# Performance work log

Hardware: AMD Instinct MI355X
Metric: run time of the kernel (lower is better)

The kernel has to match this reference:

```python
import jax, jax.numpy as jnp
import numpy as np

B, CIN, COUT, T, F = 8, 64, 64, 512, 161
KH, KW = 3, 3
PAD_H, PAD_W = 1, 1
STRIDE_H, STRIDE_W = 1, 1
DIL_H, DIL_W = 1, 1


def setup_inputs() -> dict:
    key = jax.random.key(0)
    k1, k2, k3 = jax.random.split(key, 3)
    x = jax.random.normal(k1, (B, CIN, T, F), dtype=jnp.float32)
    # kernel: [out_ch, in_ch, kernels(freq), kH, kW]
    kernel = jax.random.normal(k2, (COUT, CIN, F, KH, KW), dtype=jnp.float32) * 0.05
    bias = jax.random.normal(k3, (1, COUT, 1, F), dtype=jnp.float32) * 0.05
    return {"x": x, "kernel": kernel, "bias": bias}


def reference(x, kernel, bias):
    # Frequency-varying conv: out[b,o,t,f] = sum_{i,m,n} xp[b,i,t*sH+m*dH, f*sW+n*dW] * kernel[o,i,f,m,n] + bias
    xp = jnp.pad(x, ((0, 0), (0, 0), (PAD_H, PAD_H), (PAD_W, PAD_W)))
    Hp, Wp = xp.shape[-2], xp.shape[-1]
    out_t = (Hp - ((KH - 1) * DIL_H + 1)) // STRIDE_H + 1
    out_f = (Wp - ((KW - 1) * DIL_W + 1)) // STRIDE_W + 1  # == F == kernels
    out = jnp.zeros((x.shape[0], kernel.shape[0], out_t, out_f), dtype=x.dtype)
    # Small fixed loop over the 3x3 window; avoids materializing [B,C,T,F,3,3] patches.
    for m in range(KH):
        for n in range(KW):
            xs = xp[:, :,
                    m * DIL_H : m * DIL_H + out_t * STRIDE_H : STRIDE_H,
                    n * DIL_W : n * DIL_W + out_f * STRIDE_W : STRIDE_W]  # [B,Cin,T,F]
            out = out + jnp.einsum('bitf,oif->botf', xs, kernel[:, :, :, m, n])
    out = out + bias
    return out
```

## Files before the change

kernel.cpp:

```cpp
#include <hip/hip_runtime.h>
#include <hip/hip_bf16.h>

#define CIN   64
#define COUT  64
#define TT    512
#define FF    161
#define KTOT  576
#define TFSTR (TT*FF)
#define FP_   168

#define W2_BYTES  ((size_t)FF*COUT*KTOT*2)
#define X2_BYTES  ((size_t)8*TT*FP_*64*2)
#define TMP_BYTES ((size_t)8*FF*TT*COUT*2)
#define PW_BLOCKS 5796

typedef __bf16 bf16x8 __attribute__((ext_vector_type(8)));
typedef float  f32x4  __attribute__((ext_vector_type(4)));
typedef unsigned short u16x8 __attribute__((ext_vector_type(8)));
typedef unsigned short u16x4 __attribute__((ext_vector_type(4)));
typedef unsigned int   u32x2 __attribute__((ext_vector_type(2)));
typedef float f4u __attribute__((ext_vector_type(4), aligned(4)));

__device__ __forceinline__ unsigned short f2bf(float v) {
    union { float f; unsigned int u; } c; c.f = v;
    unsigned int u = c.u + 0x7FFFu + ((c.u >> 16) & 1u);
    return (unsigned short)(u >> 16);
}
__device__ __forceinline__ float bf2f(unsigned short h) {
    union { unsigned int u; float f; } c; c.u = (unsigned)h << 16;
    return c.f;
}

__global__ __launch_bounds__(256) void prep_fused(
    const float* __restrict__ ksrc, unsigned short* __restrict__ w2,
    const float* __restrict__ x, unsigned short* __restrict__ x2)
{
    __shared__ unsigned short Xs[64][172];
    int bx = blockIdx.x;
    int tid = threadIdx.x;

    if (bx < PW_BLOCKS) {
        int g  = bx*256 + tid;
        int f  = g / 9216;
        int j  = g - f*9216;
        int o  = j / 144;
        int r  = j - o*144;
        int q  = r >> 4;
        int i4 = (r & 15) * 4;
        u16x4 v;
        #pragma unroll
        for (int e = 0; e < 4; ++e)
            v[e] = f2bf(ksrc[((size_t)(o*64 + i4 + e)*FF + f)*9 + q]);
        *(u16x4*)&w2[(size_t)f*36864 + j*4] = v;
        return;
    }

    int bt = bx - PW_BLOCKS;
    int b  = bt >> 9;
    int t  = bt & 511;
    const float* xb = x + (size_t)b*CIN*TFSTR + (size_t)t*FF;
    #pragma unroll
    for (int k = 0; k < 11; ++k) {
        int s = tid + k*256;
        if (s < 2624) {
            int i = s / 41;
            int u = s - i*41;
            const float* p = xb + (size_t)i*TFSTR + 4*u;
            if (u < 40) {
                f4u v = *(const f4u*)p;
                u32x2 pk = { (unsigned)f2bf(v.x) | ((unsigned)f2bf(v.y) << 16),
                             (unsigned)f2bf(v.z) | ((unsigned)f2bf(v.w) << 16) };
                *(u32x2*)&Xs[i][4*u] = pk;
            } else {
                Xs[i][160] = f2bf(*p);
            }
        }
    }
    __syncthreads();
    unsigned short* ob = x2 + (size_t)bt * FP_ * 64;
    #pragma unroll
    for (int k = 0; k < 6; ++k) {
        int s = tid + k*256;
        if (s < 1344) {
            int fp = s >> 3;
            int j  = s & 7;
            u16x8 v = {0,0,0,0,0,0,0,0};
            if (fp >= 1 && fp < 162) {
                int f = fp - 1;
                #pragma unroll
                for (int e = 0; e < 8; ++e) v[e] = Xs[j*8 + e][f];
            }
            *(u16x8*)&ob[fp*64 + j*8] = v;
        }
    }
}

__global__ __launch_bounds__(256, 3) void conv_mfma7(
    const unsigned short* __restrict__ x2, const unsigned short* __restrict__ w2,
    const float* __restrict__ bias, unsigned short* __restrict__ tmp)
{
    int bx  = blockIdx.x;
    int xcd = bx & 7;
    int s   = bx >> 3;
    int fblk, g;
    if (s < 320) {
        int qd = s >> 5, w = s & 31;
        fblk = qd*4 + (w & 3);
        g    = (w >> 2)*8 + xcd;
    } else {
        fblk = 40;
        g    = (s - 320)*8 + xcd;
    }
    int b  = g >> 3;
    int t0 = (g & 7) * 64;
    int f0 = fblk * 4;

    __shared__ alignas(16) unsigned short As[2][12800];

    int tid = threadIdx.x;
    int wv  = tid >> 6;
    int l   = tid & 63;
    int l15 = l & 15;
    int lq  = l >> 4;
    int o   = wv*16 + l15;

    const unsigned short* zrow = x2 + 167*64;

    auto stage = [&](int ih) {
        #pragma unroll
        for (int it = 0; it < 7; ++it) {
            int idx = tid + it*256;
            if (idx < 1600) {
                int row = idx >> 2;
                int j   = idx & 3;
                int fl  = row / 66;
                int tl  = row - fl*66;
                int gt  = t0 - 1 + tl;
                int fp  = f0 + fl;
                bool ok = (fl < 6) && (gt >= 0) && (gt < TT);
                int key = (tl + fl) & 3;
                const unsigned short* src = ok
                    ? x2 + ((((size_t)b*TT + gt)*FP_ + fp)*64 + ih*32 + ((j ^ key) * 8))
                    : zrow + j*8;
                __builtin_amdgcn_global_load_lds(
                    (const __attribute__((address_space(1))) void*)src,
                    (__attribute__((address_space(3))) void*)(&As[ih][(size_t)(wv*64 + it*256)*8]),
                    16, 0, 0);
            }
        }
    };

    f32x4 acc[4][4] = {};
    const unsigned short* wb = w2 + ((size_t)f0*COUT + o)*KTOT;

    stage(0);
    __syncthreads();
    stage(1);

    #pragma unroll
    for (int is = 0; is < 2; ++is) {
        if (is) __syncthreads();
        const unsigned short* bp = As[is];
        int kb = is*32 + lq*8;
        #pragma unroll
        for (int dm = 0; dm < 3; ++dm) {
            bf16x8 bw[3][4];
            #pragma unroll
            for (int dn = 0; dn < 3; ++dn)
                #pragma unroll
                for (int u = 0; u < 4; ++u)
                    bw[dn][u] = *(const bf16x8*)&wb[(size_t)u*COUT*KTOT + (dm*3+dn)*64 + kb];
            #pragma unroll
            for (int mf = 0; mf < 4; ++mf) {
                int tl = mf*16 + l15 + dm;
                bf16x8 a6[6];
                #pragma unroll
                for (int v = 0; v < 6; ++v) {
                    int slot = lq ^ ((tl + v) & 3);
                    a6[v] = *(const bf16x8*)&bp[(size_t)(v*66 + tl)*32 + slot*8];
                }
                #pragma unroll
                for (int dn = 0; dn < 3; ++dn)
                    #pragma unroll
                    for (int u = 0; u < 4; ++u)
                        acc[u][mf] = __builtin_amdgcn_mfma_f32_16x16x32_bf16(
                            a6[u + dn], bw[dn][u], acc[u][mf], 0, 0, 0);
            }
        }
    }

    #pragma unroll
    for (int u = 0; u < 4; ++u) {
        int fe = f0 + u;
        if (fe < FF) {
            float bv = bias[o*FF + fe];
            size_t tb = ((size_t)b*FF + fe)*TT + t0;
            #pragma unroll
            for (int mf = 0; mf < 4; ++mf)
                #pragma unroll
                for (int rr = 0; rr < 4; ++rr) {
                    int t = mf*16 + lq*4 + rr;
                    tmp[(tb + t)*COUT + o] = f2bf(acc[u][mf][rr] + bv);
                }
        }
    }
}

__global__ __launch_bounds__(256) void finalize2(
    const unsigned short* __restrict__ tmp, float* __restrict__ out)
{
    int bx = blockIdx.x;
    int b  = bx & 7;
    int s  = bx >> 3;
    int tb = s >> 1;
    int oh = s & 1;
    int t0 = tb * 4;
    int o0 = oh * 32;

    __shared__ unsigned short Ld[644*40];

    int tid = threadIdx.x;

    #pragma unroll
    for (int k = 0; k < 11; ++k) {
        int sl = tid + k*256;
        if (sl < 2576) {
            int f = sl >> 4;
            int r = sl & 15;
            int t = r >> 2;
            int j = r & 3;
            const unsigned short* src =
                tmp + (((size_t)b*FF + f)*TT + t0 + t)*COUT + o0 + j*8;
            int row = t*FF + f;
            *(u16x8*)&Ld[row*40 + ((j ^ (f & 3)) << 3)] = *(const u16x8*)src;
        }
    }
    __syncthreads();

    for (int ol = 0; ol < 32; ++ol) {
        int o = o0 + ol;
        float* op = out + (((size_t)b*COUT + o)*TT + t0)*FF;
        int jo = ol >> 3, o7 = ol & 7;
        #pragma unroll
        for (int k = 0; k < 3; ++k) {
            int r = tid + k*256;
            if (r < 4*FF) {
                int f = r % FF;
                op[r] = bf2f(Ld[r*40 + ((jo ^ (f & 3)) << 3) + o7]);
            }
        }
    }
}

__global__ __launch_bounds__(256) void conv_mfma(
    const float* __restrict__ x, const unsigned short* __restrict__ w2,
    const float* __restrict__ bias, float* __restrict__ out)
{
    int bx = blockIdx.x;
    int r  = bx & 7;
    int q  = bx >> 3;
    int fblk = q % 41;
    int g  = (q / 41) * 8 + r;
    int b  = g >> 3;
    int t0 = (g & 7) * 64;
    int f0 = fblk * 4;

    __shared__ unsigned short Bs[6][66][64];
    int tid = threadIdx.x;

    for (int i = 0; i < 64; i += 4) {
        #pragma unroll
        for (int pp = 0; pp < 2; ++pp) {
            int p = tid + pp*256;
            if (p < 396) {
                int tl = p / 6, fl = p % 6;
                int gt = t0 - 1 + tl;
                int gf = f0 - 1 + fl;
                bool ok = (gt >= 0) && (gt < TT) && (gf >= 0) && (gf < FF);
                const float* xp = x + (((size_t)(b*CIN + i)*TT + gt)*FF + gf);
                float v0 = ok ? xp[0]       : 0.f;
                float v1 = ok ? xp[TFSTR]   : 0.f;
                float v2 = ok ? xp[2*TFSTR] : 0.f;
                float v3 = ok ? xp[3*TFSTR] : 0.f;
                int isw = i ^ (((tl + fl) & 7) << 3);
                ushort4 pk;
                pk.x = f2bf(v0); pk.y = f2bf(v1); pk.z = f2bf(v2); pk.w = f2bf(v3);
                *reinterpret_cast<ushort4*>(&Bs[fl][tl][isw]) = pk;
            }
        }
    }
    __syncthreads();

    int wv = tid >> 6;
    int l  = tid & 63;
    int f  = f0 + wv;
    if (f >= FF) return;

    int l15 = l & 15;
    int lq  = l >> 4;
    f32x4 acc[4][4] = {};
    const unsigned short* wb = w2 + (size_t)f * (COUT * KTOT);

    #pragma unroll
    for (int dm = 0; dm < 3; ++dm)
    #pragma unroll
    for (int dn = 0; dn < 3; ++dn) {
        int fl = wv + dn;
        int kq = (dm*3 + dn) * 64;
        #pragma unroll
        for (int is = 0; is < 2; ++is) {
            int i0 = is*32 + lq*8;
            bf16x8 a[4];
            #pragma unroll
            for (int mf = 0; mf < 4; ++mf) {
                int tl  = mf*16 + l15 + dm;
                int isw = i0 ^ (((tl + fl) & 7) << 3);
                a[mf] = *(const bf16x8*)&Bs[fl][tl][isw];
            }
            int kb = kq + i0;
            #pragma unroll
            for (int nf = 0; nf < 4; ++nf) {
                bf16x8 bfr = *(const bf16x8*)&wb[(size_t)(nf*16 + l15) * KTOT + kb];
                #pragma unroll
                for (int mf = 0; mf < 4; ++mf)
                    acc[mf][nf] = __builtin_amdgcn_mfma_f32_16x16x32_bf16(
                        a[mf], bfr, acc[mf][nf], 0, 0, 0);
            }
        }
    }

    #pragma unroll
    for (int nf = 0; nf < 4; ++nf) {
        int o = nf*16 + l15;
        float bv = bias[o*FF + f];
        size_t obase = (((size_t)b*COUT + o)*TT + t0 + lq*4)*FF + f;
        #pragma unroll
        for (int mf = 0; mf < 4; ++mf)
            #pragma unroll
            for (int rr = 0; rr < 4; ++rr)
                out[obase + (size_t)(mf*16 + rr)*FF] = acc[mf][nf][rr] + bv;
    }
}

extern "C" void kernel_launch(void* const* d_in, const int* in_sizes, int n_in,
                              void* d_out, int out_size, void* d_ws, size_t ws_size,
                              hipStream_t stream)
{
    (void)in_sizes; (void)n_in; (void)out_size;
    const float* x    = (const float*)d_in[0];
    const float* k    = (const float*)d_in[1];
    const float* bias = (const float*)d_in[2];
    float* out = (float*)d_out;
    unsigned short* w2  = (unsigned short*)d_ws;
    unsigned short* x2  = (unsigned short*)((char*)d_ws + W2_BYTES);
    unsigned short* tmp = (unsigned short*)((char*)d_ws + W2_BYTES + X2_BYTES);

    bool big2 = (ws_size >= W2_BYTES + X2_BYTES + TMP_BYTES);

    prep_fused<<<big2 ? (PW_BLOCKS + 8*TT) : PW_BLOCKS, 256, 0, stream>>>(k, w2, x, x2);

    if (big2) {
        conv_mfma7<<<8*328, 256, 0, stream>>>(x2, w2, bias, tmp);
        finalize2<<<2048, 256, 0, stream>>>(tmp, out);
    } else {
        conv_mfma<<<8*41*8, 256, 0, stream>>>(x, w2, bias, out);
    }
}
```

Baseline: 276.9 us.

## Shrink conv tile to two frequencies, stage full input once, double-buffer weights

The MFMA conv kernel now covers 2 frequency outputs per block instead of 4. It loads all 64 input channels for 4 padded frequencies into LDS in a single stage with an 8-way XOR swizzle, replacing the two-phase 32-channel staging. Weight fragments are double-buffered in registers across the six (channel-half, kernel-row) phases, and the launch bound rises to 4 blocks per SM. The aim is higher occupancy and less sync, and the grid grows to 5184 blocks. In exchange, the input halo reuse per block is lower, and the XCD-aware block mapping is dropped.

```diff
diff --git a/kernel.cpp b/kernel.cpp
--- a/kernel.cpp
+++ b/kernel.cpp
@@ -6,6 +6,7 @@
 #define TT    512
 #define FF    161
 #define KTOT  576
+#define WST   (COUT*KTOT)
 #define TFSTR (TT*FF)
 #define FP_   168
 
@@ -95,102 +96,95 @@
     }
 }
 
-__global__ __launch_bounds__(256, 3) void conv_mfma7(
+__global__ __launch_bounds__(256, 4) void conv_mfma8(
     const unsigned short* __restrict__ x2, const unsigned short* __restrict__ w2,
     const float* __restrict__ bias, unsigned short* __restrict__ tmp)
 {
-    int bx  = blockIdx.x;
-    int xcd = bx & 7;
-    int s   = bx >> 3;
-    int fblk, g;
-    if (s < 320) {
-        int qd = s >> 5, w = s & 31;
-        fblk = qd*4 + (w & 3);
-        g    = (w >> 2)*8 + xcd;
-    } else {
-        fblk = 40;
-        g    = (s - 320)*8 + xcd;
-    }
-    int b  = g >> 3;
-    int t0 = (g & 7) * 64;
-    int f0 = fblk * 4;
-
-    __shared__ alignas(16) unsigned short As[2][12800];
+    int bx   = blockIdx.x;
+    int b    = bx & 7;
+    int r    = bx >> 3;
+    int tq   = r & 7;
+    int fblk = r >> 3;
+    int t0   = tq * 64;
+    int f0   = fblk * 2;
+
+    __shared__ alignas(16) unsigned short As[264*64];
 
     int tid = threadIdx.x;
-    int wv  = tid >> 6;
+    int wq  = tid >> 6;
     int l   = tid & 63;
     int l15 = l & 15;
     int lq  = l >> 4;
-    int o   = wv*16 + l15;
+    int o   = wq*16 + l15;
 
     const unsigned short* zrow = x2 + 167*64;
 
-    auto stage = [&](int ih) {
-        #pragma unroll
-        for (int it = 0; it < 7; ++it) {
-            int idx = tid + it*256;
-            if (idx < 1600) {
-                int row = idx >> 2;
-                int j   = idx & 3;
-                int fl  = row / 66;
-                int tl  = row - fl*66;
-                int gt  = t0 - 1 + tl;
-                int fp  = f0 + fl;
-                bool ok = (fl < 6) && (gt >= 0) && (gt < TT);
-                int key = (tl + fl) & 3;
-                const unsigned short* src = ok
-                    ? x2 + ((((size_t)b*TT + gt)*FP_ + fp)*64 + ih*32 + ((j ^ key) * 8))
-                    : zrow + j*8;
-                __builtin_amdgcn_global_load_lds(
-                    (const __attribute__((address_space(1))) void*)src,
-                    (__attribute__((address_space(3))) void*)(&As[ih][(size_t)(wv*64 + it*256)*8]),
-                    16, 0, 0);
-            }
-        }
+    #pragma unroll
+    for (int it = 0; it < 9; ++it) {
+        int idx = tid + it*256;
+        if (idx < 2112) {
+            int row = idx >> 3;
+            int j   = idx & 7;
+            int fl  = row / 66;
+            int tl  = row - fl*66;
+            int gt  = t0 - 1 + tl;
+            int fp  = f0 + fl;
+            bool ok = (gt >= 0) && (gt < TT);
+            int key = (tl + fl) & 7;
+            const unsigned short* src = ok
+                ? x2 + ((((size_t)b*TT + gt)*FP_ + fp)*64 + ((j ^ key) * 8))
+                : zrow + j*8;
+            __builtin_amdgcn_global_load_lds(
+                (const __attribute__((address_space(1))) void*)src,
+                (__attribute__((address_space(3))) void*)(As + (size_t)idx*8),
+                16, 0, 0);
+        }
+    }
+    __syncthreads();
+
+    f32x4 acc[2][4] = {};
+    const unsigned short* wb = w2 + ((size_t)f0*COUT + o)*KTOT;
+
+    bf16x8 bw0[6], bw1[6];
+    auto ldw = [&](bf16x8 (&dst)[6], int p) {
+        int is = p / 3, dm = p - (p/3)*3;
+        int kb = is*32 + lq*8;
+        #pragma unroll
+        for (int dn = 0; dn < 3; ++dn)
+            #pragma unroll
+            for (int u = 0; u < 2; ++u)
+                dst[dn*2 + u] = *(const bf16x8*)&wb[(size_t)u*WST + (dm*3 + dn)*64 + kb];
     };
 
-    f32x4 acc[4][4] = {};
-    const unsigned short* wb = w2 + ((size_t)f0*COUT + o)*KTOT;
-
-    stage(0);
-    __syncthreads();
-    stage(1);
-
-    #pragma unroll
-    for (int is = 0; is < 2; ++is) {
-        if (is) __syncthreads();
-        const unsigned short* bp = As[is];
-        int kb = is*32 + lq*8;
-        #pragma unroll
-        for (int dm = 0; dm < 3; ++dm) {
-            bf16x8 bw[3][4];
+    ldw(bw0, 0);
+    #pragma unroll
+    for (int p = 0; p < 6; ++p) {
+        if (p < 5) {
+            if (p & 1) ldw(bw0, p + 1); else ldw(bw1, p + 1);
+        }
+        int is = p / 3, dm = p - (p/3)*3;
+        int sbase = is*4 + lq;
+        #pragma unroll
+        for (int mf = 0; mf < 4; ++mf) {
+            int tl = mf*16 + l15 + dm;
+            bf16x8 a4[4];
+            #pragma unroll
+            for (int fl = 0; fl < 4; ++fl) {
+                int slot = sbase ^ ((tl + fl) & 7);
+                a4[fl] = *(const bf16x8*)&As[(size_t)(fl*66 + tl)*64 + slot*8];
+            }
             #pragma unroll
             for (int dn = 0; dn < 3; ++dn)
                 #pragma unroll
-                for (int u = 0; u < 4; ++u)
-                    bw[dn][u] = *(const bf16x8*)&wb[(size_t)u*COUT*KTOT + (dm*3+dn)*64 + kb];
-            #pragma unroll
-            for (int mf = 0; mf < 4; ++mf) {
-                int tl = mf*16 + l15 + dm;
-                bf16x8 a6[6];
-                #pragma unroll
-                for (int v = 0; v < 6; ++v) {
-                    int slot = lq ^ ((tl + v) & 3);
-                    a6[v] = *(const bf16x8*)&bp[(size_t)(v*66 + tl)*32 + slot*8];
-                }
-                #pragma unroll
-                for (int dn = 0; dn < 3; ++dn)
-                    #pragma unroll
-                    for (int u = 0; u < 4; ++u)
-                        acc[u][mf] = __builtin_amdgcn_mfma_f32_16x16x32_bf16(
-                            a6[u + dn], bw[dn][u], acc[u][mf], 0, 0, 0);
-            }
-        }
-    }
-
-    #pragma unroll
-    for (int u = 0; u < 4; ++u) {
+                for (int u = 0; u < 2; ++u)
+                    acc[u][mf] = __builtin_amdgcn_mfma_f32_16x16x32_bf16(
+                        a4[u + dn], (p & 1) ? bw1[dn*2 + u] : bw0[dn*2 + u],
+                        acc[u][mf], 0, 0, 0);
+        }
+    }
+
+    #pragma unroll
+    for (int u = 0; u < 2; ++u) {
         int fe = f0 + u;
         if (fe < FF) {
             float bv = bias[o*FF + fe];
@@ -360,7 +354,7 @@
     prep_fused<<<big2 ? (PW_BLOCKS + 8*TT) : PW_BLOCKS, 256, 0, stream>>>(k, w2, x, x2);
 
     if (big2) {
-        conv_mfma7<<<8*328, 256, 0, stream>>>(x2, w2, bias, tmp);
+        conv_mfma8<<<5184, 256, 0, stream>>>(x2, w2, bias, tmp);
         finalize2<<<2048, 256, 0, stream>>>(tmp, out);
     } else {
         conv_mfma<<<8*41*8, 256, 0, stream>>>(x, w2, bias, out);
```

Result: faster. 261.1 us (-5.7%).
